# Kernel tuning notes

Hardware: AMD Instinct MI355X
Metric: run time of the kernel (lower is better)

Reference implementation:

```python
import jax, jax.numpy as jnp
import numpy as np


def _lsa(cost):
    """Jonker-Volgenant shortest-augmenting-path LSAP (scipy-equivalent).
    cost: np.float64 [n, m] with n <= m. Returns col4row [n] (column assigned to each row)."""
    n, m = cost.shape
    u = np.zeros(n)
    v = np.zeros(m)
    path = np.full(m, -1, dtype=np.int64)
    col4row = np.full(n, -1, dtype=np.int64)
    row4col = np.full(m, -1, dtype=np.int64)
    for cur_row in range(n):
        minv = np.full(m, np.inf)          # shortest path cost to each column
        remaining = np.ones(m, dtype=bool)  # columns not yet scanned
        SR = np.zeros(n, dtype=bool)        # scanned rows
        i = cur_row
        min_val = 0.0
        sink = -1
        while sink == -1:
            SR[i] = True
            idx = np.nonzero(remaining)[0]
            r = min_val + cost[i, idx] - u[i] - v[idx]
            better = r < minv[idx]
            bi = idx[better]
            minv[bi] = r[better]
            path[bi] = i
            j = idx[np.argmin(minv[idx])]
            min_val = minv[j]
            remaining[j] = False
            if row4col[j] == -1:
                sink = j
            else:
                i = row4col[j]
        # dual updates
        u[cur_row] += min_val
        other = SR.copy(); other[cur_row] = False
        rows = np.nonzero(other)[0]
        u[rows] += min_val - minv[col4row[rows]]
        sc = ~remaining
        v[sc] -= min_val - minv[sc]
        # augment along alternating path
        j = sink
        while True:
            i = path[j]
            row4col[j] = i
            col4row[i], j = j, col4row[i]
            if i == cur_row:
                break
    return col4row


def _valid_counts(gt_np):
    """Count of boxes before the first all-zero [2,3] box, per sample."""
    iszero = np.all(gt_np == 0, axis=(2, 3))  # [B, N]
    N = gt_np.shape[1]
    return np.where(iszero.any(axis=1), iszero.argmax(axis=1), N).astype(np.int64)


def _orderings(cost_np, counts):
    B, N, _ = cost_np.shape
    ordering = np.zeros((B, N), dtype=np.int32)
    for b in range(B):
        c = int(counts[b])
        col4row = _lsa(cost_np[b, :c])            # assign first c rows
        rest = np.setdiff1d(np.arange(N), col4row)  # unmapped columns (sorted)
        ordering[b] = np.concatenate([col4row, rest])
    return ordering


def setup_inputs() -> dict:
    key = jax.random.key(0)
    k1, k2 = jax.random.split(key)
    B, N = 256, 64
    cost = jax.random.uniform(k1, (B, N, N), dtype=jnp.float32)
    gt = np.abs(np.asarray(jax.random.normal(k2, (B, N, 2, 3), dtype=jnp.float32))) + 0.1
    counts = N - (np.arange(B) % 32)  # per-sample valid instance counts
    for b in range(B):
        gt[b, counts[b]:] = 0.0       # zero-pad invalid boxes (matches box_mask)
    return {"cost": cost, "gt_boxes": jnp.asarray(gt, dtype=jnp.float32)}


def reference(cost, gt_boxes):
    counts = _valid_counts(np.asarray(gt_boxes))
    ordering = _orderings(np.asarray(cost, dtype=np.float64), counts)
    ord_j = jnp.asarray(ordering)  # [B, N] int32
    B, N = ord_j.shape
    # row indices after concat are always arange(N), so loss = mean of cost[b, r, ordering[b, r]]
    picked = jnp.take_along_axis(cost, ord_j[:, :, None].astype(jnp.int32), axis=2)  # [B, N, 1]
    loss = picked.sum() / jnp.asarray(B * N, dtype=cost.dtype)
    return (ord_j, loss)
```

## Files before the change

### kernel.cpp

```cpp
#include <hip/hip_runtime.h>


union DU { double d; int i2[2]; };

__device__ inline double readlane_f64(double x, int l) {
    DU a; a.d = x;
    DU o;
    o.i2[0] = __builtin_amdgcn_readlane(a.i2[0], l);
    o.i2[1] = __builtin_amdgcn_readlane(a.i2[1], l);
    return o.d;
}

template <int CTRL>
__device__ inline double dpp_min_f64(double x) {
    DU a; a.d = x;
    DU b;
    b.i2[0] = __builtin_amdgcn_update_dpp(0, a.i2[0], CTRL, 0xF, 0xF, true);
    b.i2[1] = __builtin_amdgcn_update_dpp(0, a.i2[1], CTRL, 0xF, 0xF, true);
    return fmin(x, b.d);
}

__global__ __launch_bounds__(64)
void lsap_solve(const float* __restrict__ cost,
                const float* __restrict__ gt,
                float* __restrict__ out,
                double* __restrict__ partial)
{
    const int b    = blockIdx.x;
    const int lane = threadIdx.x;
    const double INF = __builtin_inf();

    __shared__ float costL[64 * 64];
    __shared__ int   ordL[64];

    const float4* cb4 = (const float4*)(cost + (size_t)b * 4096);
    float4*       cl4 = (float4*)costL;
#pragma unroll
    for (int i = 0; i < 16; ++i)
        cl4[i * 64 + lane] = cb4[i * 64 + lane];

    const float* gb = gt + (size_t)b * 384 + lane * 6;
    bool iszero = true;
#pragma unroll
    for (int k = 0; k < 6; ++k) iszero = iszero && (gb[k] == 0.0f);
    unsigned long long zmask = __ballot(iszero);
    const int c = zmask ? (__ffsll(zmask) - 1) : 64;

    double u_d = 0.0;
    double v_d = 0.0;
    int path_r    = -1;
    int row4col_r = -1;
    int col4row_r = -1;

    __syncthreads();

    for (int cur_row = 0; cur_row < c; ++cur_row) {
        double minv_d    = INF;
        bool   remaining = true;
        unsigned long long SR = 0ULL;
        int    i       = cur_row;
        double min_val = 0.0;
        int    sink    = -1;

        while (sink < 0) {
            SR |= 1ULL << i;
            const double u_i = readlane_f64(u_d, i);
            const float  cf  = costL[i * 64 + lane];
            double r = min_val + (double)cf;
            r = r - u_i;
            r = r - v_d;
            const bool upd = remaining && (r < minv_d);
            minv_d = upd ? r : minv_d;
            path_r = upd ? i : path_r;

            const double key = remaining ? minv_d : INF;
            double k = dpp_min_f64<0xB1>(key);
            k = dpp_min_f64<0x4E>(k);
            k = dpp_min_f64<0x141>(k);
            k = dpp_min_f64<0x140>(k);
            const double m0 = readlane_f64(k, 0);
            const double m1 = readlane_f64(k, 16);
            const double m2 = readlane_f64(k, 32);
            const double m3 = readlane_f64(k, 48);
            const double kmin = fmin(fmin(m0, m1), fmin(m2, m3));

            const unsigned long long eq = __ballot(key == kmin);
            const int jsel = __ffsll(eq) - 1;
            min_val   = kmin;
            remaining = remaining && (lane != jsel);
            const int rj = __builtin_amdgcn_readlane(row4col_r, jsel);
            if (rj < 0) sink = jsel; else i = rj;
        }

        {
            const bool scanned_row = (SR >> lane) & 1ULL;
            const int  gidx = col4row_r & 63;
            const double mv_g = __shfl(minv_d, gidx, 64);
            if (lane == cur_row)       u_d += min_val;
            else if (scanned_row)      u_d += min_val - mv_g;
            if (!remaining)            v_d -= min_val - minv_d;
        }

        {
            int jj = sink;
            while (true) {
                const int ii = __builtin_amdgcn_readlane(path_r, jj);
                if (lane == jj) row4col_r = ii;
                const int tmp = __builtin_amdgcn_readlane(col4row_r, ii);
                if (lane == ii) col4row_r = jj;
                jj = tmp;
                if (ii == cur_row) break;
            }
        }
    }

    const bool assigned = (row4col_r >= 0);
    const unsigned long long amask = __ballot(assigned);
    if (lane < c) ordL[lane] = col4row_r;
    if (!assigned) {
        const unsigned long long below = (~amask) & ((1ULL << lane) - 1ULL);
        ordL[c + __popcll(below)] = lane;
    }
    __syncthreads();

    const int oc = ordL[lane];
    out[b * 64 + lane] = (float)oc;

    double p = (double)costL[lane * 64 + oc];
#pragma unroll
    for (int s = 1; s < 64; s <<= 1) p += __shfl_xor(p, s, 64);
    if (lane == 0) partial[b] = p;
}

__global__ __launch_bounds__(256)
void loss_reduce(const double* __restrict__ partial, float* __restrict__ out,
                 int B)
{
    const int t = threadIdx.x;
    __shared__ double sb[4];
    double p = 0.0;
    for (int idx = t; idx < B; idx += 256) p += partial[idx];
#pragma unroll
    for (int s = 1; s < 64; s <<= 1) p += __shfl_xor(p, s, 64);
    if ((t & 63) == 0) sb[t >> 6] = p;
    __syncthreads();
    if (t == 0)
        out[B * 64] = (float)((sb[0] + sb[1] + sb[2] + sb[3]) / (double)(B * 64));
}

extern "C" void kernel_launch(void* const* d_in, const int* in_sizes, int n_in,
                              void* d_out, int out_size, void* d_ws, size_t ws_size,
                              hipStream_t stream)
{
    const float* cost = (const float*)d_in[0];
    const float* gt   = (const float*)d_in[1];
    float* out        = (float*)d_out;
    double* partial   = (double*)d_ws;

    const int B = in_sizes[0] / 4096;

    lsap_solve<<<B, 64, 0, stream>>>(cost, gt, out, partial);
    loss_reduce<<<1, 256, 0, stream>>>(partial, out, B);
}
```

Measured before the change: 115.3 us.

## Run LSAP in exact int32 arithmetic when costs lie on 2^-23 grid

Each block checks whether every cost value is an exact multiple of 2^-23 in [0,2). If so, it runs the Jonker-Volgenant solver in scaled int32 arithmetic with the cost column held in registers instead of f64 math on shared memory. Otherwise it falls back to the original f64 path. This removes double-precision arithmetic and LDS loads from the serial inner loop, which is exact for uniform float inputs but adds the grid check and extra register use.

```diff
diff --git a/kernel.cpp b/kernel.cpp
--- a/kernel.cpp
+++ b/kernel.cpp
@@ -1,5 +1,7 @@
 #include <hip/hip_runtime.h>
 
+
+typedef int i32x16 __attribute__((ext_vector_type(16)));
 
 union DU { double d; int i2[2]; };
 
@@ -20,39 +22,89 @@
     return fmin(x, b.d);
 }
 
-__global__ __launch_bounds__(64)
-void lsap_solve(const float* __restrict__ cost,
-                const float* __restrict__ gt,
-                float* __restrict__ out,
-                double* __restrict__ partial)
-{
-    const int b    = blockIdx.x;
-    const int lane = threadIdx.x;
+template <int CTRL>
+__device__ inline int dpp_min_i32(int x) {
+    const int o = __builtin_amdgcn_update_dpp(0, x, CTRL, 0xF, 0xF, true);
+    return o < x ? o : x;
+}
+
+__device__ void run_lsap_i32(const i32x16& c0, const i32x16& c1,
+                             const i32x16& c2, const i32x16& c3,
+                             int lane, int c,
+                             int& path_r, int& row4col_r, int& col4row_r)
+{
+    int u_s = 0;
+    int v_s = 0;
+
+    for (int cur_row = 0; cur_row < c; ++cur_row) {
+        int  minv_s    = 0x7FFFFFFF;
+        bool remaining = true;
+        unsigned long long SR = 0ULL;
+        int  i       = cur_row;
+        int  min_val = 0;
+        int  sink    = -1;
+
+        while (sink < 0) {
+            SR |= 1ULL << i;
+            const int u_i = __builtin_amdgcn_readlane(u_s, i);
+            const int iu  = __builtin_amdgcn_readfirstlane(i);
+            int cv;
+            if (iu < 32) cv = (iu < 16) ? c0[iu & 15] : c1[iu & 15];
+            else         cv = (iu < 48) ? c2[iu & 15] : c3[iu & 15];
+            const int r = (cv - v_s) + (min_val - u_i);
+            const bool upd = remaining && (r < minv_s);
+            minv_s = upd ? r : minv_s;
+            path_r = upd ? i : path_r;
+
+            const int key = remaining ? minv_s : 0x7FFFFFFF;
+            int k = dpp_min_i32<0xB1>(key);
+            k = dpp_min_i32<0x4E>(k);
+            k = dpp_min_i32<0x141>(k);
+            k = dpp_min_i32<0x140>(k);
+            const int m0 = __builtin_amdgcn_readlane(k, 0);
+            const int m1 = __builtin_amdgcn_readlane(k, 16);
+            const int m2 = __builtin_amdgcn_readlane(k, 32);
+            const int m3 = __builtin_amdgcn_readlane(k, 48);
+            const int ma = m0 < m1 ? m0 : m1;
+            const int mb = m2 < m3 ? m2 : m3;
+            const int gmin = ma < mb ? ma : mb;
+
+            const unsigned long long eq = __ballot(key == gmin);
+            const int jsel = __ffsll(eq) - 1;
+            min_val   = gmin;
+            remaining = remaining && (lane != jsel);
+            const int rj = __builtin_amdgcn_readlane(row4col_r, jsel);
+            if (rj < 0) sink = jsel; else i = rj;
+        }
+
+        {
+            const bool scanned_row = (SR >> lane) & 1ULL;
+            const int  gidx = col4row_r & 63;
+            const int  mv_g = __shfl(minv_s, gidx, 64);
+            if (lane == cur_row)       u_s += min_val;
+            else if (scanned_row)      u_s += min_val - mv_g;
+            if (!remaining)            v_s -= min_val - minv_s;
+        }
+
+        {
+            int jj = sink;
+            while (true) {
+                const int ii = __builtin_amdgcn_readlane(path_r, jj);
+                if (lane == jj) row4col_r = ii;
+                const int tmp = __builtin_amdgcn_readlane(col4row_r, ii);
+                if (lane == ii) col4row_r = jj;
+                jj = tmp;
+                if (ii == cur_row) break;
+            }
+        }
+    }
+}
+
+__device__ void run_lsap_f64(const float* __restrict__ costL, int lane, int c,
+                             int& path_r, int& row4col_r, int& col4row_r)
+{
     const double INF = __builtin_inf();
-
-    __shared__ float costL[64 * 64];
-    __shared__ int   ordL[64];
-
-    const float4* cb4 = (const float4*)(cost + (size_t)b * 4096);
-    float4*       cl4 = (float4*)costL;
-#pragma unroll
-    for (int i = 0; i < 16; ++i)
-        cl4[i * 64 + lane] = cb4[i * 64 + lane];
-
-    const float* gb = gt + (size_t)b * 384 + lane * 6;
-    bool iszero = true;
-#pragma unroll
-    for (int k = 0; k < 6; ++k) iszero = iszero && (gb[k] == 0.0f);
-    unsigned long long zmask = __ballot(iszero);
-    const int c = zmask ? (__ffsll(zmask) - 1) : 64;
-
-    double u_d = 0.0;
-    double v_d = 0.0;
-    int path_r    = -1;
-    int row4col_r = -1;
-    int col4row_r = -1;
-
-    __syncthreads();
+    double u_d = 0.0, v_d = 0.0;
 
     for (int cur_row = 0; cur_row < c; ++cur_row) {
         double minv_d    = INF;
@@ -83,10 +135,9 @@
             const double m2 = readlane_f64(k, 32);
             const double m3 = readlane_f64(k, 48);
             const double kmin = fmin(fmin(m0, m1), fmin(m2, m3));
-
             const unsigned long long eq = __ballot(key == kmin);
             const int jsel = __ffsll(eq) - 1;
-            min_val   = kmin;
+            min_val = kmin;
             remaining = remaining && (lane != jsel);
             const int rj = __builtin_amdgcn_readlane(row4col_r, jsel);
             if (rj < 0) sink = jsel; else i = rj;
@@ -100,7 +151,6 @@
             else if (scanned_row)      u_d += min_val - mv_g;
             if (!remaining)            v_d -= min_val - minv_d;
         }
-
         {
             int jj = sink;
             while (true) {
@@ -113,6 +163,59 @@
             }
         }
     }
+}
+
+__global__ __launch_bounds__(64)
+void lsap_solve(const float* __restrict__ cost,
+                const float* __restrict__ gt,
+                float* __restrict__ out,
+                double* __restrict__ partial)
+{
+    const int b    = blockIdx.x;
+    const int lane = threadIdx.x;
+
+    __shared__ float costL[64 * 64];
+    __shared__ int   ordL[64];
+
+    const float4* cb4 = (const float4*)(cost + (size_t)b * 4096);
+    float4*       cl4 = (float4*)costL;
+#pragma unroll
+    for (int i = 0; i < 16; ++i)
+        cl4[i * 64 + lane] = cb4[i * 64 + lane];
+
+    const float* gb = gt + (size_t)b * 384 + lane * 6;
+    bool iszero = true;
+#pragma unroll
+    for (int k = 0; k < 6; ++k) iszero = iszero && (gb[k] == 0.0f);
+    unsigned long long zmask = __ballot(iszero);
+    const int c = zmask ? (__ffsll(zmask) - 1) : 64;
+
+    __syncthreads();
+
+    i32x16 c0, c1, c2, c3;
+    bool ongrid = true;
+#pragma unroll
+    for (int k = 0; k < 16; ++k) {
+        const double h0 = (double)costL[(k     ) * 64 + lane] * 8388608.0;
+        const double h1 = (double)costL[(k + 16) * 64 + lane] * 8388608.0;
+        const double h2 = (double)costL[(k + 32) * 64 + lane] * 8388608.0;
+        const double h3 = (double)costL[(k + 48) * 64 + lane] * 8388608.0;
+        ongrid = ongrid && (h0 >= 0.0) && (h0 < 16777216.0) && (h0 == floor(h0))
+                        && (h1 >= 0.0) && (h1 < 16777216.0) && (h1 == floor(h1))
+                        && (h2 >= 0.0) && (h2 < 16777216.0) && (h2 == floor(h2))
+                        && (h3 >= 0.0) && (h3 < 16777216.0) && (h3 == floor(h3));
+        c0[k] = (int)h0; c1[k] = (int)h1; c2[k] = (int)h2; c3[k] = (int)h3;
+    }
+    const bool fast = (__ballot(ongrid) == ~0ULL);
+
+    asm volatile("" : "+v"(c0), "+v"(c1), "+v"(c2), "+v"(c3));
+
+    int path_r    = -1;
+    int row4col_r = -1;
+    int col4row_r = -1;
+
+    if (fast) run_lsap_i32(c0, c1, c2, c3, lane, c, path_r, row4col_r, col4row_r);
+    else      run_lsap_f64(costL, lane, c, path_r, row4col_r, col4row_r);
 
     const bool assigned = (row4col_r >= 0);
     const unsigned long long amask = __ballot(assigned);
```

Result: slower. 128.4 us (+11.4%).
